# Kernel optimization log

Hardware: AMD Instinct MI355X
Metric: run time of the kernel (lower is better)

## Reference

```python
import jax, jax.numpy as jnp
import numpy as np

B, C, H, W = 4, 64, 64, 64


def setup_inputs() -> dict:
    key = jax.random.key(0)
    k1, k2, k3, k4, k5 = jax.random.split(key, 5)
    return {
        "x": jax.random.normal(k1, (B, C, H, W), dtype=jnp.float32),
        "w_qkv": jax.random.normal(k2, (3 * C, C), dtype=jnp.float32) * (1.0 / np.sqrt(C)),
        "b_qkv": jax.random.normal(k3, (3 * C,), dtype=jnp.float32) * 0.02,
        "w_proj": jax.random.normal(k4, (C, C), dtype=jnp.float32) * (1.0 / np.sqrt(C)),
        "b_proj": jax.random.normal(k5, (C,), dtype=jnp.float32) * 0.02,
    }


def reference(x, w_qkv, b_qkv, w_proj, b_proj):
    b, c, h, w = x.shape
    xf = x.reshape(b, c, h * w)                                  # [B, C, N]
    # 1x1 Conv1d == per-position linear over channels
    qkv = jnp.einsum('oc,bcn->bon', w_qkv, xf) + b_qkv[None, :, None]  # [B, 3C, N]
    q, k, v = jnp.split(qkv, 3, axis=1)                          # each [B, C, N]
    scores = jnp.einsum('bcn,bcm->bnm', q, k) / (c ** 0.5)       # [B, N, N]
    attn = jax.nn.softmax(scores, axis=-1)
    out = jnp.einsum('bcm,bnm->bcn', v, attn)                    # [B, C, N]
    out = jnp.einsum('oc,bcn->bon', w_proj, out) + b_proj[None, :, None]
    return out.reshape(b, c, h, w) + x
```

## Files before the change

### kernel.cpp

```cpp
#include <hip/hip_runtime.h>

typedef __bf16 bf16x8 __attribute__((ext_vector_type(8)));
typedef __bf16 bf16x4 __attribute__((ext_vector_type(4)));
typedef __bf16 bf16x2 __attribute__((ext_vector_type(2)));
typedef float f32x4 __attribute__((ext_vector_type(4)));
typedef short s16x4 __attribute__((ext_vector_type(4)));

#define NB 4
#define NC 64
#define NN 4096
#define SPLIT 8

#define QSCALE (0.125f * 1.44269504088896340736f)

#if __has_builtin(__builtin_amdgcn_exp2f)
#define EXP2(x) __builtin_amdgcn_exp2f(x)
#else
#define EXP2(x) exp2f(x)
#endif

__global__ __launch_bounds__(256) void qkv_kernel(
    const float* __restrict__ x, const float* __restrict__ wqkv,
    const float* __restrict__ bqkv,
    __bf16* __restrict__ Qg, __bf16* __restrict__ Kg, __bf16* __restrict__ Vg)
{
  const int tid = threadIdx.x;
  const int b = blockIdx.y;
  const int z = blockIdx.z;
  const int tsel = z >> 3;
  const int obase = (z & 7) * 8;
  const int n = blockIdx.x * 512 + tid * 2;
  const float wscale = (tsel == 0) ? QSCALE : 1.0f;

  __shared__ float wsh[8 * 64];
  __shared__ float bsh[8];
  wsh[tid]       = wqkv[(tsel * 64 + obase) * 64 + tid] * wscale;
  wsh[tid + 256] = wqkv[(tsel * 64 + obase) * 64 + tid + 256] * wscale;
  if (tid < 8) bsh[tid] = bqkv[tsel * 64 + obase + tid] * wscale;
  __syncthreads();

  float xa[64], xb[64];
#pragma unroll
  for (int c = 0; c < 64; c++) {
    const float2 t = *(const float2*)&x[((size_t)(b * 64 + c)) * NN + n];
    xa[c] = t.x; xb[c] = t.y;
  }

  float aa[8], ab[8];
#pragma unroll
  for (int j = 0; j < 8; j++) { aa[j] = bsh[j]; ab[j] = bsh[j]; }
#pragma unroll
  for (int c4 = 0; c4 < 64; c4 += 4) {
#pragma unroll
    for (int j = 0; j < 8; j++) {
      const float4 wv = *(const float4*)&wsh[j * 64 + c4];
      aa[j] = fmaf(wv.x, xa[c4 + 0], aa[j]);
      aa[j] = fmaf(wv.y, xa[c4 + 1], aa[j]);
      aa[j] = fmaf(wv.z, xa[c4 + 2], aa[j]);
      aa[j] = fmaf(wv.w, xa[c4 + 3], aa[j]);
      ab[j] = fmaf(wv.x, xb[c4 + 0], ab[j]);
      ab[j] = fmaf(wv.y, xb[c4 + 1], ab[j]);
      ab[j] = fmaf(wv.z, xb[c4 + 2], ab[j]);
      ab[j] = fmaf(wv.w, xb[c4 + 3], ab[j]);
    }
  }

  if (tsel == 2) {
#pragma unroll
    for (int j = 0; j < 8; j++) {
      bf16x2 pv;
      pv[0] = (__bf16)aa[j]; pv[1] = (__bf16)ab[j];
      *(bf16x2*)(Vg + ((size_t)(b * 64 + obase + j)) * NN + n) = pv;
    }
  } else {
    __bf16* base = (tsel == 0 ? Qg : Kg);
    bf16x8 p0, p1;
#pragma unroll
    for (int j = 0; j < 8; j++) { p0[j] = (__bf16)aa[j]; p1[j] = (__bf16)ab[j]; }
    *(bf16x8*)(base + ((size_t)(b * NN + n)) * 64 + obase) = p0;
    *(bf16x8*)(base + ((size_t)(b * NN + n + 1)) * 64 + obase) = p1;
  }
}

__global__ __launch_bounds__(256) void flash_kernel(
    const __bf16* __restrict__ Q, const __bf16* __restrict__ K,
    const __bf16* __restrict__ V, const float* __restrict__ wproj,
    __bf16* __restrict__ Opart, float* __restrict__ lpart)
{
  const int b = blockIdx.y;
  const int s = blockIdx.z;
  const int tid = threadIdx.x;
  const int wave = tid >> 6;
  const int lane = tid & 63;
  const int quad = lane >> 4;
  const int l16 = lane & 15;

  __shared__ __bf16 Kt[64 * 72];
  __shared__ __bf16 Vt[64 * 72];

  const int q0 = blockIdx.x * 128 + wave * 32;

  bf16x8 qf[2][2];
#pragma unroll
  for (int qt = 0; qt < 2; qt++) {
    const __bf16* qrow = Q + ((size_t)(b * NN + q0 + qt * 16 + l16)) * 64;
    qf[qt][0] = *(const bf16x8*)(qrow + quad * 8);
    qf[qt][1] = *(const bf16x8*)(qrow + 32 + quad * 8);
  }

  f32x4 acc[2][4];
#pragma unroll
  for (int qt = 0; qt < 2; qt++)
#pragma unroll
    for (int ct = 0; ct < 4; ct++) acc[qt][ct] = (f32x4){0.f, 0.f, 0.f, 0.f};
  float l[2] = {0.f, 0.f};

  const int kbeg = s * (NN / SPLIT);
  const int kend = kbeg + (NN / SPLIT);
#pragma unroll 1
  for (int kt0 = kbeg; kt0 < kend; kt0 += 64) {
    __syncthreads();
#pragma unroll
    for (int it = 0; it < 2; it++) {
      const int chunk = tid + it * 256;
      const int row = chunk >> 3, col8 = (chunk & 7) * 8;
      *(bf16x8*)(&Kt[row * 72 + col8]) =
          *(const bf16x8*)(K + ((size_t)(b * NN + kt0 + row)) * 64 + col8);
      *(bf16x8*)(&Vt[row * 72 + col8]) =
          *(const bf16x8*)(V + ((size_t)(b * 64 + row)) * NN + kt0 + col8);
    }
    __syncthreads();

    s16x4 pk[4][2];
#pragma unroll
    for (int t = 0; t < 4; t++) {
      const bf16x8 kf0 = *(const bf16x8*)(&Kt[(t * 16 + l16) * 72 + quad * 8]);
      const bf16x8 kf1 = *(const bf16x8*)(&Kt[(t * 16 + l16) * 72 + 32 + quad * 8]);
#pragma unroll
      for (int qt = 0; qt < 2; qt++) {
        f32x4 z = (f32x4){0.f, 0.f, 0.f, 0.f};
        z = __builtin_amdgcn_mfma_f32_16x16x32_bf16(kf0, qf[qt][0], z, 0, 0, 0);
        z = __builtin_amdgcn_mfma_f32_16x16x32_bf16(kf1, qf[qt][1], z, 0, 0, 0);
        const float p0 = EXP2(z[0]), p1 = EXP2(z[1]);
        const float p2 = EXP2(z[2]), p3 = EXP2(z[3]);
        l[qt] += (p0 + p1) + (p2 + p3);
        bf16x4 pv;
        pv[0] = (__bf16)p0; pv[1] = (__bf16)p1;
        pv[2] = (__bf16)p2; pv[3] = (__bf16)p3;
        pk[t][qt] = __builtin_bit_cast(s16x4, pv);
      }
    }

#pragma unroll
    for (int kg = 0; kg < 4; kg++) {
#pragma unroll
      for (int ct = 0; ct < 4; ct++) {
        const bf16x4 va =
            *(const bf16x4*)(&Vt[(ct * 16 + l16) * 72 + kg * 16 + quad * 4]);
        const s16x4 a = __builtin_bit_cast(s16x4, va);
        acc[0][ct] = __builtin_amdgcn_mfma_f32_16x16x16bf16_1k(
            a, pk[kg][0], acc[0][ct], 0, 0, 0);
        acc[1][ct] = __builtin_amdgcn_mfma_f32_16x16x16bf16_1k(
            a, pk[kg][1], acc[1][ct], 0, 0, 0);
      }
    }
  }

#pragma unroll
  for (int qt = 0; qt < 2; qt++) {
    float lr = l[qt];
    lr += __shfl_xor(lr, 16);
    lr += __shfl_xor(lr, 32);
    if (quad == 0)
      lpart[((size_t)(s * NB + b)) * NN + q0 + qt * 16 + l16] = lr;
  }

  s16x4 ob[2][4];
#pragma unroll
  for (int qt = 0; qt < 2; qt++)
#pragma unroll
    for (int ch = 0; ch < 4; ch++) {
      bf16x4 t;
#pragma unroll
      for (int r = 0; r < 4; r++) t[r] = (__bf16)acc[qt][ch][r];
      ob[qt][ch] = __builtin_bit_cast(s16x4, t);
    }

#pragma unroll
  for (int cot = 0; cot < 4; cot++) {
    f32x4 po[2];
    po[0] = (f32x4){0.f, 0.f, 0.f, 0.f};
    po[1] = (f32x4){0.f, 0.f, 0.f, 0.f};
#pragma unroll
    for (int ch = 0; ch < 4; ch++) {
      const float4 wv =
          *(const float4*)&wproj[(cot * 16 + l16) * 64 + ch * 16 + quad * 4];
      bf16x4 wb;
      wb[0] = (__bf16)wv.x; wb[1] = (__bf16)wv.y;
      wb[2] = (__bf16)wv.z; wb[3] = (__bf16)wv.w;
      const s16x4 a = __builtin_bit_cast(s16x4, wb);
      po[0] = __builtin_amdgcn_mfma_f32_16x16x16bf16_1k(a, ob[0][ch], po[0], 0, 0, 0);
      po[1] = __builtin_amdgcn_mfma_f32_16x16x16bf16_1k(a, ob[1][ch], po[1], 0, 0, 0);
    }
#pragma unroll
    for (int qt = 0; qt < 2; qt++)
#pragma unroll
      for (int r = 0; r < 4; r++)
        Opart[(((size_t)(s * NB + b)) * 64 + cot * 16 + quad * 4 + r) * NN +
              q0 + qt * 16 + l16] = (__bf16)po[qt][r];
  }
}

__global__ __launch_bounds__(256) void combine_kernel(
    const __bf16* __restrict__ Opart, const float* __restrict__ lpart,
    const float* __restrict__ bproj, const float* __restrict__ x,
    float* __restrict__ out)
{
  const int b = blockIdx.y;
  const int n0 = blockIdx.x * 32;
  const int tid = threadIdx.x;

  __shared__ float linv[32];
  if (tid < 32) {
    float lt = 0.f;
#pragma unroll
    for (int s = 0; s < SPLIT; s++)
      lt += lpart[((size_t)(s * NB + b)) * NN + n0 + tid];
    linv[tid] = 1.0f / lt;
  }
  __syncthreads();

  const int c = tid >> 2;
  const int n8 = (tid & 3) * 8;

  float o[8];
#pragma unroll
  for (int j = 0; j < 8; j++) o[j] = 0.f;
#pragma unroll
  for (int s = 0; s < SPLIT; s++) {
    const bf16x8 v = *(const bf16x8*)(
        Opart + (((size_t)(s * NB + b)) * 64 + c) * NN + n0 + n8);
#pragma unroll
    for (int j = 0; j < 8; j++) o[j] += (float)v[j];
  }

  const float bb = bproj[c];
  const float4 li0 = *(const float4*)&linv[n8];
  const float4 li1 = *(const float4*)&linv[n8 + 4];
  const size_t base = ((size_t)(b * 64 + c)) * NN + n0 + n8;
  const float4 x0 = *(const float4*)&x[base];
  const float4 x1 = *(const float4*)&x[base + 4];
  float4 r0, r1;
  r0.x = o[0] * li0.x + bb + x0.x;  r0.y = o[1] * li0.y + bb + x0.y;
  r0.z = o[2] * li0.z + bb + x0.z;  r0.w = o[3] * li0.w + bb + x0.w;
  r1.x = o[4] * li1.x + bb + x1.x;  r1.y = o[5] * li1.y + bb + x1.y;
  r1.z = o[6] * li1.z + bb + x1.z;  r1.w = o[7] * li1.w + bb + x1.w;
  *(float4*)&out[base] = r0;
  *(float4*)&out[base + 4] = r1;
}

extern "C" void kernel_launch(void* const* d_in, const int* in_sizes, int n_in,
                              void* d_out, int out_size, void* d_ws, size_t ws_size,
                              hipStream_t stream) {
  const float* x     = (const float*)d_in[0];
  const float* wqkv  = (const float*)d_in[1];
  const float* bqkv  = (const float*)d_in[2];
  const float* wproj = (const float*)d_in[3];
  const float* bproj = (const float*)d_in[4];
  float* out = (float*)d_out;

  char* ws = (char*)d_ws;
  __bf16* Q     = (__bf16*)(ws);
  __bf16* K     = (__bf16*)(ws + (2u << 20));
  __bf16* V     = (__bf16*)(ws + (4u << 20));
  __bf16* Opart = (__bf16*)(ws + (6u << 20));
  float*  lpart = (float*)(ws + (23u << 20));

  qkv_kernel<<<dim3(8, NB, 24), 256, 0, stream>>>(x, wqkv, bqkv, Q, K, V);
  flash_kernel<<<dim3(32, NB, SPLIT), 256, 0, stream>>>(Q, K, V, wproj,
                                                        Opart, lpart);
  combine_kernel<<<dim3(128, NB), 256, 0, stream>>>(Opart, lpart, bproj, x,
                                                    out);
}
```

Before: 115.1 us.

## Compute QKV projection with bf16 MFMA instead of scalar FP32 FMAs

Rewrites the QKV projection kernel to use 16x16x32 bf16 MFMA instructions. Weights are loaded directly into register fragments, with no shared-memory staging, and the grid changes from 768 blocks that each compute 8 output channels to 384 blocks that each compute all 64 channels of one of Q/K/V. This removes the heavy scalar FMA work and the repeated x reads across the 24 z-slices. In exchange, x and the weights are rounded to bf16 before the matmul, which lowers precision, and the Q/K stores become scattered 2-byte writes.

```diff
diff --git a/kernel.cpp b/kernel.cpp
--- a/kernel.cpp
+++ b/kernel.cpp
@@ -2,7 +2,6 @@
 
 typedef __bf16 bf16x8 __attribute__((ext_vector_type(8)));
 typedef __bf16 bf16x4 __attribute__((ext_vector_type(4)));
-typedef __bf16 bf16x2 __attribute__((ext_vector_type(2)));
 typedef float f32x4 __attribute__((ext_vector_type(4)));
 typedef short s16x4 __attribute__((ext_vector_type(4)));
 
@@ -25,60 +24,74 @@
     __bf16* __restrict__ Qg, __bf16* __restrict__ Kg, __bf16* __restrict__ Vg)
 {
   const int tid = threadIdx.x;
+  const int wave = tid >> 6;
+  const int lane = tid & 63;
+  const int quad = lane >> 4;
+  const int l16 = lane & 15;
   const int b = blockIdx.y;
-  const int z = blockIdx.z;
-  const int tsel = z >> 3;
-  const int obase = (z & 7) * 8;
-  const int n = blockIdx.x * 512 + tid * 2;
+  const int tsel = blockIdx.z;
+  const int n0 = blockIdx.x * 128 + wave * 32;
   const float wscale = (tsel == 0) ? QSCALE : 1.0f;
 
-  __shared__ float wsh[8 * 64];
-  __shared__ float bsh[8];
-  wsh[tid]       = wqkv[(tsel * 64 + obase) * 64 + tid] * wscale;
-  wsh[tid + 256] = wqkv[(tsel * 64 + obase) * 64 + tid + 256] * wscale;
-  if (tid < 8) bsh[tid] = bqkv[tsel * 64 + obase + tid] * wscale;
-  __syncthreads();
-
-  float xa[64], xb[64];
-#pragma unroll
-  for (int c = 0; c < 64; c++) {
-    const float2 t = *(const float2*)&x[((size_t)(b * 64 + c)) * NN + n];
-    xa[c] = t.x; xb[c] = t.y;
-  }
-
-  float aa[8], ab[8];
-#pragma unroll
-  for (int j = 0; j < 8; j++) { aa[j] = bsh[j]; ab[j] = bsh[j]; }
-#pragma unroll
-  for (int c4 = 0; c4 < 64; c4 += 4) {
-#pragma unroll
-    for (int j = 0; j < 8; j++) {
-      const float4 wv = *(const float4*)&wsh[j * 64 + c4];
-      aa[j] = fmaf(wv.x, xa[c4 + 0], aa[j]);
-      aa[j] = fmaf(wv.y, xa[c4 + 1], aa[j]);
-      aa[j] = fmaf(wv.z, xa[c4 + 2], aa[j]);
-      aa[j] = fmaf(wv.w, xa[c4 + 3], aa[j]);
-      ab[j] = fmaf(wv.x, xb[c4 + 0], ab[j]);
-      ab[j] = fmaf(wv.y, xb[c4 + 1], ab[j]);
-      ab[j] = fmaf(wv.z, xb[c4 + 2], ab[j]);
-      ab[j] = fmaf(wv.w, xb[c4 + 3], ab[j]);
-    }
-  }
-
-  if (tsel == 2) {
-#pragma unroll
-    for (int j = 0; j < 8; j++) {
-      bf16x2 pv;
-      pv[0] = (__bf16)aa[j]; pv[1] = (__bf16)ab[j];
-      *(bf16x2*)(Vg + ((size_t)(b * 64 + obase + j)) * NN + n) = pv;
-    }
-  } else {
-    __bf16* base = (tsel == 0 ? Qg : Kg);
-    bf16x8 p0, p1;
-#pragma unroll
-    for (int j = 0; j < 8; j++) { p0[j] = (__bf16)aa[j]; p1[j] = (__bf16)ab[j]; }
-    *(bf16x8*)(base + ((size_t)(b * NN + n)) * 64 + obase) = p0;
-    *(bf16x8*)(base + ((size_t)(b * NN + n + 1)) * 64 + obase) = p1;
+  bf16x8 wf[4][2];
+#pragma unroll
+  for (int ot = 0; ot < 4; ot++) {
+#pragma unroll
+    for (int ch = 0; ch < 2; ch++) {
+      const float* wp =
+          wqkv + (size_t)(tsel * 64 + ot * 16 + l16) * 64 + ch * 32 + quad * 8;
+      const float4 w0 = *(const float4*)wp;
+      const float4 w1 = *(const float4*)(wp + 4);
+      bf16x8 f;
+      f[0] = (__bf16)(w0.x * wscale); f[1] = (__bf16)(w0.y * wscale);
+      f[2] = (__bf16)(w0.z * wscale); f[3] = (__bf16)(w0.w * wscale);
+      f[4] = (__bf16)(w1.x * wscale); f[5] = (__bf16)(w1.y * wscale);
+      f[6] = (__bf16)(w1.z * wscale); f[7] = (__bf16)(w1.w * wscale);
+      wf[ot][ch] = f;
+    }
+  }
+  float bv[4];
+#pragma unroll
+  for (int ot = 0; ot < 4; ot++)
+    bv[ot] = bqkv[tsel * 64 + ot * 16 + l16] * wscale;
+
+#pragma unroll
+  for (int nt = 0; nt < 2; nt++) {
+    const int nb = n0 + nt * 16 + l16;
+
+    bf16x8 xf[2];
+#pragma unroll
+    for (int ch = 0; ch < 2; ch++) {
+      float v[8];
+#pragma unroll
+      for (int j = 0; j < 8; j++)
+        v[j] = x[(size_t)(b * 64 + ch * 32 + quad * 8 + j) * NN + nb];
+      bf16x8 f;
+#pragma unroll
+      for (int j = 0; j < 8; j++) f[j] = (__bf16)v[j];
+      xf[ch] = f;
+    }
+
+#pragma unroll
+    for (int ot = 0; ot < 4; ot++) {
+      f32x4 acc = (f32x4){bv[ot], bv[ot], bv[ot], bv[ot]};
+      acc = __builtin_amdgcn_mfma_f32_16x16x32_bf16(xf[0], wf[ot][0], acc, 0, 0, 0);
+      acc = __builtin_amdgcn_mfma_f32_16x16x32_bf16(xf[1], wf[ot][1], acc, 0, 0, 0);
+
+      if (tsel < 2) {
+        __bf16* dst = (tsel == 0) ? Qg : Kg;
+#pragma unroll
+        for (int r = 0; r < 4; r++)
+          dst[(size_t)(b * NN + n0 + nt * 16 + quad * 4 + r) * 64 + ot * 16 + l16] =
+              (__bf16)acc[r];
+      } else {
+        bf16x4 pv;
+#pragma unroll
+        for (int r = 0; r < 4; r++) pv[r] = (__bf16)acc[r];
+        *(bf16x4*)(Vg + (size_t)(b * 64 + ot * 16 + l16) * NN +
+                   n0 + nt * 16 + quad * 4) = pv;
+      }
+    }
   }
 }
 
@@ -276,7 +289,7 @@
   __bf16* Opart = (__bf16*)(ws + (6u << 20));
   float*  lpart = (float*)(ws + (23u << 20));
 
-  qkv_kernel<<<dim3(8, NB, 24), 256, 0, stream>>>(x, wqkv, bqkv, Q, K, V);
+  qkv_kernel<<<dim3(32, NB, 3), 256, 0, stream>>>(x, wqkv, bqkv, Q, K, V);
   flash_kernel<<<dim3(32, NB, SPLIT), 256, 0, stream>>>(Q, K, V, wproj,
                                                         Opart, lpart);
   combine_kernel<<<dim3(128, NB), 256, 0, stream>>>(Opart, lpart, bproj, x,
```

New measurement: 113.5 us. No clear change (-1.5%).
